# Performance work log

Measured on AMD Instinct MI355X. Metric: run time of the kernel, lower is better.

Reference implementation:

```python
import jax, jax.numpy as jnp
import numpy as np

NUM_USERS = 100000
NUM_ITEMS = 50000
EMB_DIM = 64
N_LAYERS = 3
NUM_BICLIQUES = 20000
E_ADJ = 1200000
E_HV = 400000
E_HU = 400000


def setup_inputs() -> dict:
    key = jax.random.key(0)
    ks = jax.random.split(key, 11)
    N = NUM_USERS + NUM_ITEMS
    return {
        "user_emb": jax.random.normal(ks[0], (NUM_USERS, EMB_DIM), dtype=jnp.float32) * 0.1,
        "item_emb": jax.random.normal(ks[1], (NUM_ITEMS, EMB_DIM), dtype=jnp.float32) * 0.1,
        "adj_val": jax.random.uniform(ks[2], (E_ADJ,), dtype=jnp.float32),
        "hv_val": jax.random.uniform(ks[3], (E_HV,), dtype=jnp.float32),
        "hu_val": jax.random.uniform(ks[4], (E_HU,), dtype=jnp.float32),
        "adj_row": jax.random.randint(ks[5], (E_ADJ,), 0, N, dtype=jnp.int32),
        "adj_col": jax.random.randint(ks[6], (E_ADJ,), 0, N, dtype=jnp.int32),
        "hv_row": jax.random.randint(ks[7], (E_HV,), 0, NUM_BICLIQUES, dtype=jnp.int32),
        "hv_col": jax.random.randint(ks[8], (E_HV,), 0, NUM_ITEMS, dtype=jnp.int32),
        "hu_row": jax.random.randint(ks[9], (E_HU,), 0, NUM_USERS, dtype=jnp.int32),
        "hu_col": jax.random.randint(ks[10], (E_HU,), 0, NUM_BICLIQUES, dtype=jnp.int32),
    }


def _spmm(row, col, val, x, n_rows):
    # sparse [n_rows, n_cols] @ dense [n_cols, d] via gather + segment-sum
    return jax.ops.segment_sum(val[:, None] * x[col], row, num_segments=n_rows)


def _row_degree(row, val, n_rows):
    deg = jax.ops.segment_sum(val, row, num_segments=n_rows)
    return jnp.where(deg == 0, 1.0, deg)  # matches degree[degree == 0] = 1.0


def reference(user_emb, item_emb, adj_val, hv_val, hu_val,
              adj_row, adj_col, hv_row, hv_col, hu_row, hu_col):
    N = user_emb.shape[0] + item_emb.shape[0]
    # ---- LightGCN global encoder: mean over layer embeddings ----
    all_emb = jnp.concatenate([user_emb, item_emb], axis=0)  # [N, d]
    acc = all_emb
    e = all_emb
    for _ in range(N_LAYERS):
        e = _spmm(adj_row, adj_col, adj_val, e, N)
        acc = acc + e
    final = acc / (N_LAYERS + 1)
    u_global = final[: user_emb.shape[0]]
    i_global = final[user_emb.shape[0]:]
    # ---- Biclique local encoder ----
    biclique_feat = _spmm(hv_row, hv_col, hv_val, item_emb, NUM_BICLIQUES)  # [B, d]
    biclique_feat = biclique_feat / _row_degree(hv_row, hv_val, NUM_BICLIQUES)[:, None]
    u_local = _spmm(hu_row, hu_col, hu_val, biclique_feat, user_emb.shape[0])  # [U, d]
    u_local = u_local / _row_degree(hu_row, hu_val, user_emb.shape[0])[:, None]
    return (u_global + u_local, i_global)
```

## Files before the change

kernel.cpp:

```cpp
#include <hip/hip_runtime.h>

#define NUSERS 100000
#define NITEMS 50000
#define NTOT   150000
#define NBIC   20000
#define DIM    64

#define HV_BASE  NTOT
#define HU_BASE  (NTOT + NBIC)
#define NROWS_ALL (NTOT + NBIC + NUSERS)

#define ADJ_RPB  500
#define NB_ADJ   300
#define HV_RPB   200
#define NB_HV    100
#define HU_RPB   1000
#define NB_HU    100
#define NBKT     (NB_ADJ + NB_HV + NB_HU)
#define HSIZE    512

#define EDGE_CAP 5120
#define ROWS_CAP 1024
#define NCLS     64
#define CHUNK    8192
#define PA_BLK   1024
#define PB_BLK   512

typedef _Float16 h8 __attribute__((ext_vector_type(8)));

__device__ __forceinline__ void bucket_of(int r, int& b, int& rl) {
    if (r < NTOT)          { int q = r / ADJ_RPB;               b = q;                rl = r - q * ADJ_RPB; }
    else if (r < HU_BASE)  { int rr = r - HV_BASE; int q = rr / HV_RPB;
                             b = NB_ADJ + q;                    rl = rr - q * HV_RPB; }
    else                   { int rr = r - HU_BASE; int q = rr / HU_RPB;
                             b = NB_ADJ + NB_HV + q;            rl = rr - q * HU_RPB; }
}

__global__ void to_half_kernel(const float* __restrict__ user,
                               const float* __restrict__ item,
                               _Float16* __restrict__ x16) {
    int i = blockIdx.x * blockDim.x + threadIdx.x;
    const int n8 = NTOT * DIM / 8;
    if (i >= n8) return;
    const int u8 = NUSERS * DIM / 8;
    const float4* src = (i < u8) ? (const float4*)user + 2 * (size_t)i
                                 : (const float4*)item + 2 * (size_t)(i - u8);
    float4 a = src[0], b = src[1];
    h8 h;
    h[0] = (_Float16)a.x; h[1] = (_Float16)a.y; h[2] = (_Float16)a.z; h[3] = (_Float16)a.w;
    h[4] = (_Float16)b.x; h[5] = (_Float16)b.y; h[6] = (_Float16)b.z; h[7] = (_Float16)b.w;
    ((h8*)x16)[i] = h;
}

__global__ void __launch_bounds__(PA_BLK)
phaseA_kernel(const int* __restrict__ adj_row, const int* __restrict__ adj_col,
              const float* __restrict__ adj_val,
              const int* __restrict__ hv_row, const int* __restrict__ hv_col,
              const float* __restrict__ hv_val,
              const int* __restrict__ hu_row, const int* __restrict__ hu_col,
              const float* __restrict__ hu_val,
              int* __restrict__ bkt_cnt, int2* __restrict__ tmp,
              int e_adj, int e_hv, int e_hu) {
    __shared__ int hist[HSIZE];
    __shared__ int lstart[HSIZE];
    __shared__ int destB[HSIZE];
    __shared__ int psum[HSIZE];
    __shared__ int2 stage[CHUNK];

    const int tid = threadIdx.x;
    const int e_all = e_adj + e_hv + e_hu;
    const int base = blockIdx.x * CHUNK;
    const int nloc = min(CHUNK, e_all - base);

    if (tid < HSIZE) hist[tid] = 0;
    __syncthreads();

    for (int i = tid; i < nloc; i += PA_BLK) {
        int t = base + i, r;
        if (t < e_adj)             r = adj_row[t];
        else if (t < e_adj + e_hv) r = HV_BASE + hv_row[t - e_adj];
        else                       r = HU_BASE + hu_row[t - e_adj - e_hv];
        int b, rl; bucket_of(r, b, rl);
        atomicAdd(&hist[b], 1);
    }
    __syncthreads();

    int v = 0;
    if (tid < HSIZE) { v = hist[tid]; psum[tid] = v; }
    __syncthreads();
    for (int off = 1; off < HSIZE; off <<= 1) {
        int t = 0;
        if (tid < HSIZE && tid >= off) t = psum[tid - off];
        __syncthreads();
        if (tid < HSIZE) psum[tid] += t;
        __syncthreads();
    }
    if (tid < HSIZE) lstart[tid] = psum[tid] - v;
    __syncthreads();

    if (tid < NBKT) {
        int c = hist[tid];
        if (c > 0)
            destB[tid] = tid * EDGE_CAP + atomicAdd(&bkt_cnt[tid], c) - lstart[tid];
    }
    __syncthreads();
    if (tid < HSIZE) hist[tid] = lstart[tid];
    __syncthreads();

    for (int i = tid; i < nloc; i += PA_BLK) {
        int t = base + i, r, c; float v2;
        if (t < e_adj)             { r = adj_row[t]; c = adj_col[t]; v2 = adj_val[t]; }
        else if (t < e_adj + e_hv) { int k = t - e_adj;
                                     r = HV_BASE + hv_row[k]; c = hv_col[k]; v2 = hv_val[k]; }
        else                       { int k = t - e_adj - e_hv;
                                     r = HU_BASE + hu_row[k]; c = hu_col[k]; v2 = hu_val[k]; }
        int b, rl; bucket_of(r, b, rl);
        int p = atomicAdd(&hist[b], 1);
        stage[p] = make_int2(c | (rl << 18), __float_as_int(v2));
    }
    __syncthreads();

    const int wave = tid >> 6, lane = tid & 63;
    for (int b = wave; b < NBKT; b += (PA_BLK / 64)) {
        int s = lstart[b];
        int e = hist[b];
        int d = destB[b];
        for (int j = s + lane; j < e; j += 64)
            tmp[d + j] = stage[j];
    }
}

__global__ void bkt_scan(const int* __restrict__ cnt, int* __restrict__ base) {
    __shared__ int s[HSIZE];
    int tid = threadIdx.x;
    int v = (tid < NBKT) ? cnt[tid] : 0;
    s[tid] = v;
    __syncthreads();
    for (int off = 1; off < HSIZE; off <<= 1) {
        int t = (tid >= off) ? s[tid - off] : 0;
        __syncthreads();
        s[tid] += t;
        __syncthreads();
    }
    if (tid < NBKT) base[tid] = s[tid] - v;
}

__global__ void __launch_bounds__(PB_BLK)
phaseB_kernel(const int* __restrict__ bkt_cnt, const int* __restrict__ bkt_base,
              const int2* __restrict__ tmp, int2* __restrict__ edges,
              int* __restrict__ start, int* __restrict__ cntArr,
              int* __restrict__ perm) {
    __shared__ int  rh[ROWS_CAP];
    __shared__ int  rs[ROWS_CAP];
    __shared__ int  psum[PB_BLK];
    __shared__ int  clsh[NCLS];
    __shared__ int  clsb[NCLS];
    __shared__ int2 stage[EDGE_CAP];

    const int tid = threadIdx.x;
    const int b = blockIdx.x;
    int rlo, nR;
    if (b < NB_ADJ)              { rlo = b * ADJ_RPB;                          nR = ADJ_RPB; }
    else if (b < NB_ADJ + NB_HV) { rlo = HV_BASE + (b - NB_ADJ) * HV_RPB;      nR = HV_RPB; }
    else                         { rlo = HU_BASE + (b - NB_ADJ - NB_HV) * HU_RPB; nR = HU_RPB; }

    const int nE = bkt_cnt[b];
    const int gbase = bkt_base[b];
    const int2* src = tmp + (size_t)b * EDGE_CAP;

    rh[tid] = 0;
    rh[tid + PB_BLK] = 0;
    if (tid < NCLS) clsh[tid] = 0;
    __syncthreads();

    for (int i = tid; i < nE; i += PB_BLK) {
        int2 e = src[i];
        atomicAdd(&rh[((unsigned)e.x) >> 18], 1);
    }
    __syncthreads();

    int a0 = rh[2 * tid], a1 = rh[2 * tid + 1];
    int tot = a0 + a1;
    psum[tid] = tot;
    __syncthreads();
    for (int off = 1; off < PB_BLK; off <<= 1) {
        int v = (tid >= off) ? psum[tid - off] : 0;
        __syncthreads();
        psum[tid] += v;
        __syncthreads();
    }
    int ex = psum[tid] - tot;
    rs[2 * tid]     = ex;
    rs[2 * tid + 1] = ex + a0;
    __syncthreads();

    for (int i = tid; i < nR; i += PB_BLK) {
        start[rlo + i]  = gbase + rs[i];
        cntArr[rlo + i] = rh[i];
        atomicAdd(&clsh[min(rh[i], NCLS - 1)], 1);
    }
    __syncthreads();

    if (tid < NCLS) clsb[tid] = clsh[tid];
    __syncthreads();
    for (int off = 1; off < NCLS; off <<= 1) {
        int v = 0;
        if (tid < NCLS && tid >= off) v = clsb[tid - off];
        __syncthreads();
        if (tid < NCLS) clsb[tid] += v;
        __syncthreads();
    }
    if (tid < NCLS) clsb[tid] -= clsh[tid];
    __syncthreads();

    for (int i = tid; i < nR; i += PB_BLK) {
        int cls = min(rh[i], NCLS - 1);
        int pos = atomicAdd(&clsb[cls], 1);
        perm[rlo + pos] = rlo + i;
    }
    __syncthreads();

    for (int i = tid; i < nE; i += PB_BLK) {
        int2 e = src[i];
        int rl = ((unsigned)e.x) >> 18;
        int p = atomicAdd(&rs[rl], 1);
        stage[p] = make_int2(e.x & 0x3FFFF, e.y);
    }
    __syncthreads();
    for (int i = tid; i < nE; i += PB_BLK) edges[gbase + i] = stage[i];
}

__device__ __forceinline__ void gather_row(const int2* __restrict__ edges,
                                           const _Float16* __restrict__ x,
                                           int s, int n, int c, float* acc) {
    float acc1[8] = {0.f, 0.f, 0.f, 0.f, 0.f, 0.f, 0.f, 0.f};
    int j = s, e = s + n;
    for (; j + 1 < e; j += 2) {
        int2 e0 = edges[j], e1 = edges[j + 1];
        float v0 = __int_as_float(e0.y), v1 = __int_as_float(e1.y);
        h8 x0 = *(const h8*)(x + (size_t)e0.x * DIM + c);
        h8 x1 = *(const h8*)(x + (size_t)e1.x * DIM + c);
        #pragma unroll
        for (int k = 0; k < 8; ++k) { acc[k] += v0 * (float)x0[k]; acc1[k] += v1 * (float)x1[k]; }
    }
    if (j < e) {
        int2 e0 = edges[j];
        float v0 = __int_as_float(e0.y);
        h8 x0 = *(const h8*)(x + (size_t)e0.x * DIM + c);
        #pragma unroll
        for (int k = 0; k < 8; ++k) acc[k] += v0 * (float)x0[k];
    }
    #pragma unroll
    for (int k = 0; k < 8; ++k) acc[k] += acc1[k];
}

__global__ void gatherK1(const int* __restrict__ start, const int* __restrict__ cnt,
                         const int2* __restrict__ edges, const int* __restrict__ perm,
                         const _Float16* __restrict__ X16,
                         _Float16* __restrict__ T0, _Float16* __restrict__ bic,
                         int gA) {
    int c = (threadIdx.x & 7) << 3;
    int lrow = threadIdx.x >> 3;
    if (blockIdx.x < gA) {
        int gid = blockIdx.x * 32 + lrow;
        if (gid >= NTOT) return;
        int r = perm[gid];
        float acc[8] = {0.f, 0.f, 0.f, 0.f, 0.f, 0.f, 0.f, 0.f};
        gather_row(edges, X16, start[r], cnt[r], c, acc);
        h8 o;
        #pragma unroll
        for (int k = 0; k < 8; ++k) o[k] = (_Float16)acc[k];
        *(h8*)(T0 + (size_t)r * DIM + c) = o;
    } else {
        int gid = (blockIdx.x - gA) * 32 + lrow;
        if (gid >= NBIC) return;
        int r = perm[HV_BASE + gid];
        int s = start[r], n = cnt[r];
        float acc[8] = {0.f, 0.f, 0.f, 0.f, 0.f, 0.f, 0.f, 0.f};
        gather_row(edges, X16 + (size_t)NUSERS * DIM, s, n, c, acc);
        float deg = 0.f;
        for (int j = s; j < s + n; ++j) deg += __int_as_float(edges[j].y);
        if (deg == 0.f) deg = 1.f;
        float inv = 1.f / deg;
        h8 o;
        #pragma unroll
        for (int k = 0; k < 8; ++k) o[k] = (_Float16)(acc[k] * inv);
        *(h8*)(bic + (size_t)(r - HV_BASE) * DIM + c) = o;
    }
}

__global__ void gatherK2(const int* __restrict__ start, const int* __restrict__ cnt,
                         const int2* __restrict__ edges, const int* __restrict__ perm,
                         const _Float16* __restrict__ T0, const _Float16* __restrict__ bic,
                         _Float16* __restrict__ T1, _Float16* __restrict__ ulocal,
                         int gA) {
    int c = (threadIdx.x & 7) << 3;
    int lrow = threadIdx.x >> 3;
    if (blockIdx.x < gA) {
        int gid = blockIdx.x * 32 + lrow;
        if (gid >= NTOT) return;
        int r = perm[gid];
        float acc[8] = {0.f, 0.f, 0.f, 0.f, 0.f, 0.f, 0.f, 0.f};
        gather_row(edges, T0, start[r], cnt[r], c, acc);
        h8 o;
        #pragma unroll
        for (int k = 0; k < 8; ++k) o[k] = (_Float16)acc[k];
        *(h8*)(T1 + (size_t)r * DIM + c) = o;
    } else {
        int gid = (blockIdx.x - gA) * 32 + lrow;
        if (gid >= NUSERS) return;
        int r = perm[HU_BASE + gid];
        int s = start[r], n = cnt[r];
        float acc[8] = {0.f, 0.f, 0.f, 0.f, 0.f, 0.f, 0.f, 0.f};
        gather_row(edges, bic, s, n, c, acc);
        float deg = 0.f;
        for (int j = s; j < s + n; ++j) deg += __int_as_float(edges[j].y);
        if (deg == 0.f) deg = 1.f;
        float inv = 1.f / deg;
        h8 o;
        #pragma unroll
        for (int k = 0; k < 8; ++k) o[k] = (_Float16)(acc[k] * inv);
        *(h8*)(ulocal + (size_t)(r - HU_BASE) * DIM + c) = o;
    }
}

__global__ void gatherK3(const int* __restrict__ start, const int* __restrict__ cnt,
                         const int2* __restrict__ edges, const int* __restrict__ perm,
                         const _Float16* __restrict__ X16,
                         const _Float16* __restrict__ T0,
                         const _Float16* __restrict__ T1,
                         const _Float16* __restrict__ ulocal,
                         float* __restrict__ out) {
    int gid = blockIdx.x * 32 + (threadIdx.x >> 3);
    if (gid >= NTOT) return;
    int c = (threadIdx.x & 7) << 3;
    int r = perm[gid];
    float acc[8] = {0.f, 0.f, 0.f, 0.f, 0.f, 0.f, 0.f, 0.f};
    gather_row(edges, T1, start[r], cnt[r], c, acc);
    size_t o = (size_t)r * DIM + c;
    h8 x0 = *(const h8*)(X16 + o);
    h8 t0 = *(const h8*)(T0 + o);
    h8 t1 = *(const h8*)(T1 + o);
    float rr[8];
    #pragma unroll
    for (int k = 0; k < 8; ++k)
        rr[k] = 0.25f * ((float)x0[k] + (float)t0[k] + (float)t1[k] + acc[k]);
    if (r < NUSERS) {
        h8 ul = *(const h8*)(ulocal + o);
        #pragma unroll
        for (int k = 0; k < 8; ++k) rr[k] += (float)ul[k];
    }
    float4 lo = make_float4(rr[0], rr[1], rr[2], rr[3]);
    float4 hi = make_float4(rr[4], rr[5], rr[6], rr[7]);
    float4* op = (float4*)(out + o);
    op[0] = lo;
    op[1] = hi;
}

extern "C" void kernel_launch(void* const* d_in, const int* in_sizes, int n_in,
                              void* d_out, int out_size, void* d_ws, size_t ws_size,
                              hipStream_t stream) {
    const float* user_emb = (const float*)d_in[0];
    const float* item_emb = (const float*)d_in[1];
    const float* adj_val  = (const float*)d_in[2];
    const float* hv_val   = (const float*)d_in[3];
    const float* hu_val   = (const float*)d_in[4];
    const int*   adj_row  = (const int*)d_in[5];
    const int*   adj_col  = (const int*)d_in[6];
    const int*   hv_row   = (const int*)d_in[7];
    const int*   hv_col   = (const int*)d_in[8];
    const int*   hu_row   = (const int*)d_in[9];
    const int*   hu_col   = (const int*)d_in[10];

    const int E_ADJ = in_sizes[2];
    const int E_HV  = in_sizes[3];
    const int E_HU  = in_sizes[4];
    const int E_ALL = E_ADJ + E_HV + E_HU;

    char* ws = (char*)d_ws;
    auto alloc = [&](size_t bytes) -> char* {
        char* p = ws;
        ws += (bytes + 255) & ~(size_t)255;
        return p;
    };
    const size_t SZ_H = (size_t)NTOT * DIM * sizeof(_Float16);
    _Float16* X16     = (_Float16*)alloc(SZ_H);
    _Float16* T0      = (_Float16*)alloc(SZ_H);
    _Float16* T1      = (_Float16*)alloc(SZ_H);
    _Float16* bic     = (_Float16*)alloc((size_t)NBIC * DIM * sizeof(_Float16));
    _Float16* ulocal  = (_Float16*)alloc((size_t)NUSERS * DIM * sizeof(_Float16));
    int*   cnt      = (int*)alloc((size_t)NROWS_ALL * sizeof(int));
    int*   start    = (int*)alloc((size_t)NROWS_ALL * sizeof(int));
    int*   perm     = (int*)alloc((size_t)NROWS_ALL * sizeof(int));
    int2*  edges    = (int2*)alloc((size_t)E_ALL * sizeof(int2));
    int2*  tmp      = (int2*)alloc((size_t)NBKT * EDGE_CAP * sizeof(int2));
    int*   bkt_cnt  = (int*)alloc(NBKT * sizeof(int));
    int*   bkt_base = (int*)alloc(NBKT * sizeof(int));

    const int BLK = 256;
    auto cdiv = [](int a, int b) { return (a + b - 1) / b; };

    hipMemsetAsync(bkt_cnt, 0, NBKT * sizeof(int), stream);
    phaseA_kernel<<<cdiv(E_ALL, CHUNK), PA_BLK, 0, stream>>>(adj_row, adj_col, adj_val,
                                                             hv_row, hv_col, hv_val,
                                                             hu_row, hu_col, hu_val,
                                                             bkt_cnt, tmp, E_ADJ, E_HV, E_HU);
    to_half_kernel<<<cdiv(NTOT * DIM / 8, BLK), BLK, 0, stream>>>(user_emb, item_emb, X16);
    bkt_scan<<<1, HSIZE, 0, stream>>>(bkt_cnt, bkt_base);
    phaseB_kernel<<<NBKT, PB_BLK, 0, stream>>>(bkt_cnt, bkt_base, tmp, edges,
                                               start, cnt, perm);

    const int gA  = cdiv(NTOT, 32);
    const int gHV = cdiv(NBIC, 32);
    const int gHU = cdiv(NUSERS, 32);

    gatherK1<<<gA + gHV, BLK, 0, stream>>>(start, cnt, edges, perm, X16, T0, bic, gA);
    gatherK2<<<gA + gHU, BLK, 0, stream>>>(start, cnt, edges, perm, T0, bic, T1, ulocal, gA);
    gatherK3<<<gA, BLK, 0, stream>>>(start, cnt, edges, perm, X16, T0, T1, ulocal,
                                     (float*)d_out);
}
```

Baseline: 276.2 us.

## Fuse preprocessing kernels, drop degree-sorted row permutation, unroll gather by four

Folds the fp16 conversion into the bucketing kernel as a grid-stride tail, and moves the bucket prefix scan into each phaseB block so the separate scan kernel disappears. Removes the per-bucket degree-class permutation, so gather kernels walk rows in natural order instead of load-balanced order. Unrolls the edge gather to four edges per iteration and computes the row degree in the same pass, removing the second edge loop for the biclique rows. In exchange, warps may see more imbalance between rows of different lengths, and every phaseB block now repeats the 500-entry scan.

```diff
diff --git a/kernel.cpp b/kernel.cpp
--- a/kernel.cpp
+++ b/kernel.cpp
@@ -21,7 +21,6 @@
 
 #define EDGE_CAP 5120
 #define ROWS_CAP 1024
-#define NCLS     64
 #define CHUNK    8192
 #define PA_BLK   1024
 #define PB_BLK   512
@@ -34,22 +33,6 @@
                              b = NB_ADJ + q;                    rl = rr - q * HV_RPB; }
     else                   { int rr = r - HU_BASE; int q = rr / HU_RPB;
                              b = NB_ADJ + NB_HV + q;            rl = rr - q * HU_RPB; }
-}
-
-__global__ void to_half_kernel(const float* __restrict__ user,
-                               const float* __restrict__ item,
-                               _Float16* __restrict__ x16) {
-    int i = blockIdx.x * blockDim.x + threadIdx.x;
-    const int n8 = NTOT * DIM / 8;
-    if (i >= n8) return;
-    const int u8 = NUSERS * DIM / 8;
-    const float4* src = (i < u8) ? (const float4*)user + 2 * (size_t)i
-                                 : (const float4*)item + 2 * (size_t)(i - u8);
-    float4 a = src[0], b = src[1];
-    h8 h;
-    h[0] = (_Float16)a.x; h[1] = (_Float16)a.y; h[2] = (_Float16)a.z; h[3] = (_Float16)a.w;
-    h[4] = (_Float16)b.x; h[5] = (_Float16)b.y; h[6] = (_Float16)b.z; h[7] = (_Float16)b.w;
-    ((h8*)x16)[i] = h;
 }
 
 __global__ void __launch_bounds__(PA_BLK)
@@ -59,6 +42,8 @@
               const float* __restrict__ hv_val,
               const int* __restrict__ hu_row, const int* __restrict__ hu_col,
               const float* __restrict__ hu_val,
+              const float* __restrict__ user, const float* __restrict__ item,
+              _Float16* __restrict__ x16,
               int* __restrict__ bkt_cnt, int2* __restrict__ tmp,
               int e_adj, int e_hv, int e_hu) {
     __shared__ int hist[HSIZE];
@@ -128,33 +113,28 @@
         for (int j = s + lane; j < e; j += 64)
             tmp[d + j] = stage[j];
     }
-}
-
-__global__ void bkt_scan(const int* __restrict__ cnt, int* __restrict__ base) {
-    __shared__ int s[HSIZE];
-    int tid = threadIdx.x;
-    int v = (tid < NBKT) ? cnt[tid] : 0;
-    s[tid] = v;
-    __syncthreads();
-    for (int off = 1; off < HSIZE; off <<= 1) {
-        int t = (tid >= off) ? s[tid - off] : 0;
-        __syncthreads();
-        s[tid] += t;
-        __syncthreads();
-    }
-    if (tid < NBKT) base[tid] = s[tid] - v;
+
+    const int n8 = NTOT * DIM / 8;
+    const int u8 = NUSERS * DIM / 8;
+    const int gsz = gridDim.x * PA_BLK;
+    for (int i = blockIdx.x * PA_BLK + tid; i < n8; i += gsz) {
+        const float4* src = (i < u8) ? (const float4*)user + 2 * (size_t)i
+                                     : (const float4*)item + 2 * (size_t)(i - u8);
+        float4 a = src[0], b = src[1];
+        h8 h;
+        h[0] = (_Float16)a.x; h[1] = (_Float16)a.y; h[2] = (_Float16)a.z; h[3] = (_Float16)a.w;
+        h[4] = (_Float16)b.x; h[5] = (_Float16)b.y; h[6] = (_Float16)b.z; h[7] = (_Float16)b.w;
+        ((h8*)x16)[i] = h;
+    }
 }
 
 __global__ void __launch_bounds__(PB_BLK)
-phaseB_kernel(const int* __restrict__ bkt_cnt, const int* __restrict__ bkt_base,
+phaseB_kernel(const int* __restrict__ bkt_cnt,
               const int2* __restrict__ tmp, int2* __restrict__ edges,
-              int* __restrict__ start, int* __restrict__ cntArr,
-              int* __restrict__ perm) {
+              int* __restrict__ start, int* __restrict__ cntArr) {
     __shared__ int  rh[ROWS_CAP];
     __shared__ int  rs[ROWS_CAP];
     __shared__ int  psum[PB_BLK];
-    __shared__ int  clsh[NCLS];
-    __shared__ int  clsb[NCLS];
     __shared__ int2 stage[EDGE_CAP];
 
     const int tid = threadIdx.x;
@@ -165,12 +145,22 @@
     else                         { rlo = HU_BASE + (b - NB_ADJ - NB_HV) * HU_RPB; nR = HU_RPB; }
 
     const int nE = bkt_cnt[b];
-    const int gbase = bkt_base[b];
+
+    int bv = (tid < NBKT) ? bkt_cnt[tid] : 0;
+    psum[tid] = bv;
+    __syncthreads();
+    for (int off = 1; off < PB_BLK; off <<= 1) {
+        int t = (tid >= off) ? psum[tid - off] : 0;
+        __syncthreads();
+        psum[tid] += t;
+        __syncthreads();
+    }
+    const int gbase = psum[b] - nE;
+
     const int2* src = tmp + (size_t)b * EDGE_CAP;
 
     rh[tid] = 0;
     rh[tid + PB_BLK] = 0;
-    if (tid < NCLS) clsh[tid] = 0;
     __syncthreads();
 
     for (int i = tid; i < nE; i += PB_BLK) {
@@ -197,26 +187,6 @@
     for (int i = tid; i < nR; i += PB_BLK) {
         start[rlo + i]  = gbase + rs[i];
         cntArr[rlo + i] = rh[i];
-        atomicAdd(&clsh[min(rh[i], NCLS - 1)], 1);
-    }
-    __syncthreads();
-
-    if (tid < NCLS) clsb[tid] = clsh[tid];
-    __syncthreads();
-    for (int off = 1; off < NCLS; off <<= 1) {
-        int v = 0;
-        if (tid < NCLS && tid >= off) v = clsb[tid - off];
-        __syncthreads();
-        if (tid < NCLS) clsb[tid] += v;
-        __syncthreads();
-    }
-    if (tid < NCLS) clsb[tid] -= clsh[tid];
-    __syncthreads();
-
-    for (int i = tid; i < nR; i += PB_BLK) {
-        int cls = min(rh[i], NCLS - 1);
-        int pos = atomicAdd(&clsb[cls], 1);
-        perm[rlo + pos] = rlo + i;
     }
     __syncthreads();
 
@@ -230,41 +200,50 @@
     for (int i = tid; i < nE; i += PB_BLK) edges[gbase + i] = stage[i];
 }
 
-__device__ __forceinline__ void gather_row(const int2* __restrict__ edges,
-                                           const _Float16* __restrict__ x,
-                                           int s, int n, int c, float* acc) {
+__device__ __forceinline__ float gather_row(const int2* __restrict__ edges,
+                                            const _Float16* __restrict__ x,
+                                            int s, int n, int c, float* acc) {
     float acc1[8] = {0.f, 0.f, 0.f, 0.f, 0.f, 0.f, 0.f, 0.f};
+    float ds = 0.f;
     int j = s, e = s + n;
-    for (; j + 1 < e; j += 2) {
-        int2 e0 = edges[j], e1 = edges[j + 1];
+    for (; j + 3 < e; j += 4) {
+        int2 e0 = edges[j], e1 = edges[j + 1], e2 = edges[j + 2], e3 = edges[j + 3];
         float v0 = __int_as_float(e0.y), v1 = __int_as_float(e1.y);
+        float v2 = __int_as_float(e2.y), v3 = __int_as_float(e3.y);
         h8 x0 = *(const h8*)(x + (size_t)e0.x * DIM + c);
         h8 x1 = *(const h8*)(x + (size_t)e1.x * DIM + c);
-        #pragma unroll
-        for (int k = 0; k < 8; ++k) { acc[k] += v0 * (float)x0[k]; acc1[k] += v1 * (float)x1[k]; }
-    }
-    if (j < e) {
+        h8 x2 = *(const h8*)(x + (size_t)e2.x * DIM + c);
+        h8 x3 = *(const h8*)(x + (size_t)e3.x * DIM + c);
+        ds += (v0 + v1) + (v2 + v3);
+        #pragma unroll
+        for (int k = 0; k < 8; ++k) {
+            acc[k]  += v0 * (float)x0[k] + v2 * (float)x2[k];
+            acc1[k] += v1 * (float)x1[k] + v3 * (float)x3[k];
+        }
+    }
+    for (; j < e; ++j) {
         int2 e0 = edges[j];
         float v0 = __int_as_float(e0.y);
         h8 x0 = *(const h8*)(x + (size_t)e0.x * DIM + c);
+        ds += v0;
         #pragma unroll
         for (int k = 0; k < 8; ++k) acc[k] += v0 * (float)x0[k];
     }
     #pragma unroll
     for (int k = 0; k < 8; ++k) acc[k] += acc1[k];
+    return ds;
 }
 
 __global__ void gatherK1(const int* __restrict__ start, const int* __restrict__ cnt,
-                         const int2* __restrict__ edges, const int* __restrict__ perm,
+                         const int2* __restrict__ edges,
                          const _Float16* __restrict__ X16,
                          _Float16* __restrict__ T0, _Float16* __restrict__ bic,
                          int gA) {
     int c = (threadIdx.x & 7) << 3;
     int lrow = threadIdx.x >> 3;
     if (blockIdx.x < gA) {
-        int gid = blockIdx.x * 32 + lrow;
-        if (gid >= NTOT) return;
-        int r = perm[gid];
+        int r = blockIdx.x * 32 + lrow;
+        if (r >= NTOT) return;
         float acc[8] = {0.f, 0.f, 0.f, 0.f, 0.f, 0.f, 0.f, 0.f};
         gather_row(edges, X16, start[r], cnt[r], c, acc);
         h8 o;
@@ -272,34 +251,30 @@
         for (int k = 0; k < 8; ++k) o[k] = (_Float16)acc[k];
         *(h8*)(T0 + (size_t)r * DIM + c) = o;
     } else {
-        int gid = (blockIdx.x - gA) * 32 + lrow;
-        if (gid >= NBIC) return;
-        int r = perm[HV_BASE + gid];
-        int s = start[r], n = cnt[r];
+        int g = (blockIdx.x - gA) * 32 + lrow;
+        if (g >= NBIC) return;
+        int r = HV_BASE + g;
         float acc[8] = {0.f, 0.f, 0.f, 0.f, 0.f, 0.f, 0.f, 0.f};
-        gather_row(edges, X16 + (size_t)NUSERS * DIM, s, n, c, acc);
-        float deg = 0.f;
-        for (int j = s; j < s + n; ++j) deg += __int_as_float(edges[j].y);
+        float deg = gather_row(edges, X16 + (size_t)NUSERS * DIM, start[r], cnt[r], c, acc);
         if (deg == 0.f) deg = 1.f;
         float inv = 1.f / deg;
         h8 o;
         #pragma unroll
         for (int k = 0; k < 8; ++k) o[k] = (_Float16)(acc[k] * inv);
-        *(h8*)(bic + (size_t)(r - HV_BASE) * DIM + c) = o;
+        *(h8*)(bic + (size_t)g * DIM + c) = o;
     }
 }
 
 __global__ void gatherK2(const int* __restrict__ start, const int* __restrict__ cnt,
-                         const int2* __restrict__ edges, const int* __restrict__ perm,
+                         const int2* __restrict__ edges,
                          const _Float16* __restrict__ T0, const _Float16* __restrict__ bic,
                          _Float16* __restrict__ T1, _Float16* __restrict__ ulocal,
                          int gA) {
     int c = (threadIdx.x & 7) << 3;
     int lrow = threadIdx.x >> 3;
     if (blockIdx.x < gA) {
-        int gid = blockIdx.x * 32 + lrow;
-        if (gid >= NTOT) return;
-        int r = perm[gid];
+        int r = blockIdx.x * 32 + lrow;
+        if (r >= NTOT) return;
         float acc[8] = {0.f, 0.f, 0.f, 0.f, 0.f, 0.f, 0.f, 0.f};
         gather_row(edges, T0, start[r], cnt[r], c, acc);
         h8 o;
@@ -307,34 +282,30 @@
         for (int k = 0; k < 8; ++k) o[k] = (_Float16)acc[k];
         *(h8*)(T1 + (size_t)r * DIM + c) = o;
     } else {
-        int gid = (blockIdx.x - gA) * 32 + lrow;
-        if (gid >= NUSERS) return;
-        int r = perm[HU_BASE + gid];
-        int s = start[r], n = cnt[r];
+        int g = (blockIdx.x - gA) * 32 + lrow;
+        if (g >= NUSERS) return;
+        int r = HU_BASE + g;
         float acc[8] = {0.f, 0.f, 0.f, 0.f, 0.f, 0.f, 0.f, 0.f};
-        gather_row(edges, bic, s, n, c, acc);
-        float deg = 0.f;
-        for (int j = s; j < s + n; ++j) deg += __int_as_float(edges[j].y);
+        float deg = gather_row(edges, bic, start[r], cnt[r], c, acc);
         if (deg == 0.f) deg = 1.f;
         float inv = 1.f / deg;
         h8 o;
         #pragma unroll
         for (int k = 0; k < 8; ++k) o[k] = (_Float16)(acc[k] * inv);
-        *(h8*)(ulocal + (size_t)(r - HU_BASE) * DIM + c) = o;
+        *(h8*)(ulocal + (size_t)g * DIM + c) = o;
     }
 }
 
 __global__ void gatherK3(const int* __restrict__ start, const int* __restrict__ cnt,
-                         const int2* __restrict__ edges, const int* __restrict__ perm,
+                         const int2* __restrict__ edges,
                          const _Float16* __restrict__ X16,
                          const _Float16* __restrict__ T0,
                          const _Float16* __restrict__ T1,
                          const _Float16* __restrict__ ulocal,
                          float* __restrict__ out) {
-    int gid = blockIdx.x * 32 + (threadIdx.x >> 3);
-    if (gid >= NTOT) return;
+    int r = blockIdx.x * 32 + (threadIdx.x >> 3);
+    if (r >= NTOT) return;
     int c = (threadIdx.x & 7) << 3;
-    int r = perm[gid];
     float acc[8] = {0.f, 0.f, 0.f, 0.f, 0.f, 0.f, 0.f, 0.f};
     gather_row(edges, T1, start[r], cnt[r], c, acc);
     size_t o = (size_t)r * DIM + c;
@@ -391,11 +362,9 @@
     _Float16* ulocal  = (_Float16*)alloc((size_t)NUSERS * DIM * sizeof(_Float16));
     int*   cnt      = (int*)alloc((size_t)NROWS_ALL * sizeof(int));
     int*   start    = (int*)alloc((size_t)NROWS_ALL * sizeof(int));
-    int*   perm     = (int*)alloc((size_t)NROWS_ALL * sizeof(int));
     int2*  edges    = (int2*)alloc((size_t)E_ALL * sizeof(int2));
     int2*  tmp      = (int2*)alloc((size_t)NBKT * EDGE_CAP * sizeof(int2));
     int*   bkt_cnt  = (int*)alloc(NBKT * sizeof(int));
-    int*   bkt_base = (int*)alloc(NBKT * sizeof(int));
 
     const int BLK = 256;
     auto cdiv = [](int a, int b) { return (a + b - 1) / b; };
@@ -404,18 +373,16 @@
     phaseA_kernel<<<cdiv(E_ALL, CHUNK), PA_BLK, 0, stream>>>(adj_row, adj_col, adj_val,
                                                              hv_row, hv_col, hv_val,
                                                              hu_row, hu_col, hu_val,
+                                                             user_emb, item_emb, X16,
                                                              bkt_cnt, tmp, E_ADJ, E_HV, E_HU);
-    to_half_kernel<<<cdiv(NTOT * DIM / 8, BLK), BLK, 0, stream>>>(user_emb, item_emb, X16);
-    bkt_scan<<<1, HSIZE, 0, stream>>>(bkt_cnt, bkt_base);
-    phaseB_kernel<<<NBKT, PB_BLK, 0, stream>>>(bkt_cnt, bkt_base, tmp, edges,
-                                               start, cnt, perm);
+    phaseB_kernel<<<NBKT, PB_BLK, 0, stream>>>(bkt_cnt, tmp, edges, start, cnt);
 
     const int gA  = cdiv(NTOT, 32);
     const int gHV = cdiv(NBIC, 32);
     const int gHU = cdiv(NUSERS, 32);
 
-    gatherK1<<<gA + gHV, BLK, 0, stream>>>(start, cnt, edges, perm, X16, T0, bic, gA);
-    gatherK2<<<gA + gHU, BLK, 0, stream>>>(start, cnt, edges, perm, T0, bic, T1, ulocal, gA);
-    gatherK3<<<gA, BLK, 0, stream>>>(start, cnt, edges, perm, X16, T0, T1, ulocal,
+    gatherK1<<<gA + gHV, BLK, 0, stream>>>(start, cnt, edges, X16, T0, bic, gA);
+    gatherK2<<<gA + gHU, BLK, 0, stream>>>(start, cnt, edges, T0, bic, T1, ulocal, gA);
+    gatherK3<<<gA, BLK, 0, stream>>>(start, cnt, edges, X16, T0, T1, ulocal,
                                      (float*)d_out);
 }
```

Result: faster. 253.7 us (-8.1%).
